# Kernel optimization log

Hardware: AMD Instinct MI355X
Metric: run time of the kernel (lower is better)

## Reference

```python
import jax, jax.numpy as jnp
import numpy as np

R_DISC = 0.05  # radius for discrepancy indicator
R_SIM = 0.03   # radius for sim/cross (indicator computed but unused downstream, as in source)
EPS = 1e-9


def setup_inputs() -> dict:
    key = jax.random.key(0)
    k1, k2, k3, k4 = jax.random.split(key, 4)
    bz, N, nsmp, K, C = 32, 16384, 4096, 64, 6
    features = jax.random.normal(k1, (bz, N, C), dtype=jnp.float32)
    nearest_k_idx = jax.random.randint(k2, (bz, nsmp, K), 0, N)
    # distances in [0, 0.06) so roughly half fall within r=0.03/0.05
    nearest_k_dist = jax.random.uniform(k3, (bz, nsmp, K), dtype=jnp.float32) * 0.06
    fps_idx = jax.random.randint(k4, (bz * nsmp,), 0, bz * N)
    return {"features": features, "nearest_k_idx": nearest_k_idx,
            "nearest_k_dist": nearest_k_dist, "fps_idx": fps_idx}


def _batched_index_select(features, idx):
    # features [bz,N,C], idx [bz,nsmp,K] -> [bz,nsmp,K,C]
    return jax.vmap(lambda f, i: f[i])(features, idx)


def _cos_sim_avg(feat_sub, nk_feat):
    # feat_sub [bz,nsmp,d], nk_feat [bz,nsmp,K,d] -> [bz,nsmp,1]
    num = jnp.sum(feat_sub[:, :, None, :] * nk_feat, axis=-1)
    den = jnp.maximum(jnp.linalg.norm(feat_sub, axis=-1)[:, :, None]
                      * jnp.linalg.norm(nk_feat, axis=-1), EPS)
    return jnp.mean(num / den, axis=-1, keepdims=True)


def reference(features, nearest_k_idx, nearest_k_dist, fps_idx):
    bz, N, C = features.shape
    nsmp = nearest_k_idx.shape[1]
    nk = _batched_index_select(features, nearest_k_idx)          # [bz,nsmp,K,C]
    feats_sub = features.reshape(bz * N, C)[fps_idx].reshape(bz, nsmp, C)

    # --- generate_feature_discrepancy (r=0.05): masked weighted neighbor mean ---
    ind = (nearest_k_dist <= R_DISC).astype(features.dtype)[..., None]  # [bz,nsmp,K,1]
    nk_avg = jnp.sum(nk * ind, axis=2) / jnp.sum(ind, axis=2)
    discrepancy = feats_sub - nk_avg                              # [bz,nsmp,C]

    # --- generate_feature_sim (r=0.03): mean cosine sim on xyz and normal splits ---
    sim = jnp.concatenate([_cos_sim_avg(feats_sub[:, :, :3], nk[:, :, :, :3]),
                           _cos_sim_avg(feats_sub[:, :, 3:], nk[:, :, :, 3:])],
                          axis=-1)                                # [bz,nsmp,2]

    # --- generate_feature_cross_prod: mean of feat_sub x neighbor over K ---
    cross = jnp.cross(feats_sub[:, :, None, :3], nk[:, :, :, :3])  # [bz,nsmp,K,3]
    cross_avg = jnp.mean(cross, axis=2)                            # [bz,nsmp,3]

    return jnp.concatenate([discrepancy, sim, cross_avg], axis=-1)  # [bz,nsmp,C+5]
```

## Files before the change

kernel.cpp:

```cpp
#include <hip/hip_runtime.h>

#define BZ    32
#define NPTS  16384
#define NSMP  4096
#define KNB   64
#define NCH   6
#define RDISC 0.05f


__global__ __launch_bounds__(64) void pnpp_kernel(
    const float* __restrict__ feat,
    const int*   __restrict__ nk_idx,
    const float* __restrict__ nk_dist,
    const int*   __restrict__ fps_idx,
    float*       __restrict__ out)
{
    const int lane = threadIdx.x & 63;
    const int bid  = blockIdx.x;
    const int work = (bid & 7) * (gridDim.x >> 3) + (bid >> 3);
    const int g = lane >> 2;
    const int j = lane & 3;
    const int s = work * 16 + g;
    const int b = s >> 12;

    const int p = fps_idx[s];
    const float* fsrow = feat + (long)p * NCH;
    const float4 fa  = *(const float4*)(fsrow);
    const float2 fb2 = *(const float2*)(fsrow + 4);
    const float fs0=fa.x, fs1=fa.y, fs2=fa.z, fs3=fa.w, fs4=fb2.x, fs5=fb2.y;
    const float qs1 = fs0*fs0 + fs1*fs1 + fs2*fs2;
    const float qs2 = fs3*fs3 + fs4*fs4 + fs5*fs5;

    const float* fbase = feat + (long)b * (NPTS * NCH);

    float cnt=0.f;
    float s0=0.f,s1=0.f,s2=0.f,s3=0.f,s4=0.f,s5=0.f;
    float m0=0.f,m1=0.f,m2=0.f;
    float c1=0.f,c2=0.f;

    const long kb0 = (long)s * KNB + j * 4;
    #pragma unroll
    for (int c = 0; c < 4; ++c) {
        const int4   i4 = *(const int4*)  (nk_idx  + kb0 + c * 16);
        const float4 d4 = *(const float4*)(nk_dist + kb0 + c * 16);
        const int   ridx[4] = {i4.x, i4.y, i4.z, i4.w};
        const float rdst[4] = {d4.x, d4.y, d4.z, d4.w};
        #pragma unroll
        for (int q = 0; q < 4; ++q) {
            const float* fr = fbase + (long)ridx[q] * NCH;
            const float4 fA = *(const float4*)(fr);
            const float2 fB = *(const float2*)(fr + 4);
            const float f0=fA.x, f1=fA.y, f2=fA.z, f3=fA.w, f4=fB.x, f5=fB.y;

            const float ind = (rdst[q] <= RDISC) ? 1.f : 0.f;
            cnt += ind;
            s0 += ind*f0; s1 += ind*f1; s2 += ind*f2;
            s3 += ind*f3; s4 += ind*f4; s5 += ind*f5;
            m0 += f0; m1 += f1; m2 += f2;

            const float q1 = f0*f0 + f1*f1 + f2*f2;
            const float n1 = fs0*f0 + fs1*f1 + fs2*f2;
            c1 += n1 * __builtin_amdgcn_rsqf(qs1 * q1);

            const float q2 = f3*f3 + f4*f4 + f5*f5;
            const float n2 = fs3*f3 + fs4*f4 + fs5*f5;
            c2 += n2 * __builtin_amdgcn_rsqf(qs2 * q2);
        }
    }

    #pragma unroll
    for (int m = 1; m < 4; m <<= 1) {
        cnt += __shfl_xor(cnt, m, 64);
        s0  += __shfl_xor(s0,  m, 64);
        s1  += __shfl_xor(s1,  m, 64);
        s2  += __shfl_xor(s2,  m, 64);
        s3  += __shfl_xor(s3,  m, 64);
        s4  += __shfl_xor(s4,  m, 64);
        s5  += __shfl_xor(s5,  m, 64);
        m0  += __shfl_xor(m0,  m, 64);
        m1  += __shfl_xor(m1,  m, 64);
        m2  += __shfl_xor(m2,  m, 64);
        c1  += __shfl_xor(c1,  m, 64);
        c2  += __shfl_xor(c2,  m, 64);
    }

    const float rc = __builtin_amdgcn_rcpf(cnt);
    const float d0 = fs0 - s0*rc, d1 = fs1 - s1*rc, d2 = fs2 - s2*rc;
    const float d3 = fs3 - s3*rc, d4 = fs4 - s4*rc, d5 = fs5 - s5*rc;
    const float ik = 1.f / (float)KNB;
    const float o6 = c1 * ik, o7 = c2 * ik;
    const float mm0 = m0 * ik, mm1 = m1 * ik, mm2 = m2 * ik;
    const float o8  = fs1*mm2 - fs2*mm1;
    const float o9  = fs2*mm0 - fs0*mm2;
    const float o10 = fs0*mm1 - fs1*mm0;

    const float v0 = (j==0) ? d0 : (j==1) ? d1 : (j==2) ? d2 : d3;
    const float v1 = (j==0) ? d4 : (j==1) ? d5 : (j==2) ? o6 : o7;
    const float v2 = (j==0) ? o8 : (j==1) ? o9 : o10;
    float* orow = out + (long)s * 11;
    orow[j]     = v0;
    orow[4 + j] = v1;
    if (j < 3) orow[8 + j] = v2;
}

extern "C" void kernel_launch(void* const* d_in, const int* in_sizes, int n_in,
                              void* d_out, int out_size, void* d_ws, size_t ws_size,
                              hipStream_t stream) {
    const float* feat = (const float*)d_in[0];
    const int*   nki  = (const int*)  d_in[1];
    const float* nkd  = (const float*)d_in[2];
    const int*   fps  = (const int*)  d_in[3];
    float* out = (float*)d_out;

    const int total_samples = BZ * NSMP;
    const int blocks = total_samples / 16;
    pnpp_kernel<<<dim3(blocks), dim3(64), 0, stream>>>(feat, nki, nkd, fps, out);
}
```

Baseline: 54.41 us.

## Split each neighbor row across lane pairs with single float4 gathers

Each sample now uses 8 lanes instead of 4. Lane pairs split the 6-channel neighbor row: the even lane loads channels 0-3 and the odd lane loads channels 2-5, each with one float4 gather, replacing a float4 plus float2 per lane, and each lane computes one of the two cosine terms. Results are rebuilt with extra xor shuffles. Blocks grow to 256 threads (4 waves) and index math moves from 64-bit to 32-bit. This halves per-lane gather and ALU work and doubles lane-level parallelism, at the cost of redundant loads of channels 2-3 and more shuffles.

```diff
diff --git a/kernel.cpp b/kernel.cpp
--- a/kernel.cpp
+++ b/kernel.cpp
@@ -8,7 +8,7 @@
 #define RDISC 0.05f
 
 
-__global__ __launch_bounds__(64) void pnpp_kernel(
+__global__ __launch_bounds__(256) void pnpp_kernel(
     const float* __restrict__ feat,
     const int*   __restrict__ nk_idx,
     const float* __restrict__ nk_dist,
@@ -16,91 +16,117 @@
     float*       __restrict__ out)
 {
     const int lane = threadIdx.x & 63;
+    const int wid  = threadIdx.x >> 6;
     const int bid  = blockIdx.x;
     const int work = (bid & 7) * (gridDim.x >> 3) + (bid >> 3);
-    const int g = lane >> 2;
-    const int j = lane & 3;
-    const int s = work * 16 + g;
+    const int g      = lane >> 3;
+    const int t      = lane & 7;
+    const int h      = t >> 1;
+    const int parity = t & 1;
+    const int s = work * 32 + wid * 8 + g;
     const int b = s >> 12;
 
     const int p = fps_idx[s];
-    const float* fsrow = feat + (long)p * NCH;
+    const float* fsrow = feat + p * NCH;
     const float4 fa  = *(const float4*)(fsrow);
     const float2 fb2 = *(const float2*)(fsrow + 4);
     const float fs0=fa.x, fs1=fa.y, fs2=fa.z, fs3=fa.w, fs4=fb2.x, fs5=fb2.y;
     const float qs1 = fs0*fs0 + fs1*fs1 + fs2*fs2;
     const float qs2 = fs3*fs3 + fs4*fs4 + fs5*fs5;
 
-    const float* fbase = feat + (long)b * (NPTS * NCH);
+    const float g0 = parity ? fs3 : fs0;
+    const float g1 = parity ? fs4 : fs1;
+    const float g2 = parity ? fs5 : fs2;
+    const float qsel = parity ? qs2 : qs1;
+
+    const float* fbase = feat + b * (NPTS * NCH) + parity * 2;
 
     float cnt=0.f;
-    float s0=0.f,s1=0.f,s2=0.f,s3=0.f,s4=0.f,s5=0.f;
-    float m0=0.f,m1=0.f,m2=0.f;
-    float c1=0.f,c2=0.f;
+    float A=0.f, B=0.f, C=0.f, D=0.f;
+    float mx=0.f, my=0.f, mz=0.f;
+    float cc=0.f;
 
-    const long kb0 = (long)s * KNB + j * 4;
+    const int kb = s * KNB + h * 16;
     #pragma unroll
     for (int c = 0; c < 4; ++c) {
-        const int4   i4 = *(const int4*)  (nk_idx  + kb0 + c * 16);
-        const float4 d4 = *(const float4*)(nk_dist + kb0 + c * 16);
+        const int4   i4 = *(const int4*)  (nk_idx  + kb + c * 4);
+        const float4 d4 = *(const float4*)(nk_dist + kb + c * 4);
         const int   ridx[4] = {i4.x, i4.y, i4.z, i4.w};
         const float rdst[4] = {d4.x, d4.y, d4.z, d4.w};
         #pragma unroll
         for (int q = 0; q < 4; ++q) {
-            const float* fr = fbase + (long)ridx[q] * NCH;
-            const float4 fA = *(const float4*)(fr);
-            const float2 fB = *(const float2*)(fr + 4);
-            const float f0=fA.x, f1=fA.y, f2=fA.z, f3=fA.w, f4=fB.x, f5=fB.y;
-
+            const float4 v = *(const float4*)(fbase + ridx[q] * NCH);
             const float ind = (rdst[q] <= RDISC) ? 1.f : 0.f;
             cnt += ind;
-            s0 += ind*f0; s1 += ind*f1; s2 += ind*f2;
-            s3 += ind*f3; s4 += ind*f4; s5 += ind*f5;
-            m0 += f0; m1 += f1; m2 += f2;
+            A += ind*v.x; B += ind*v.y; C += ind*v.z; D += ind*v.w;
+            mx += v.x; my += v.y; mz += v.z;
 
-            const float q1 = f0*f0 + f1*f1 + f2*f2;
-            const float n1 = fs0*f0 + fs1*f1 + fs2*f2;
-            c1 += n1 * __builtin_amdgcn_rsqf(qs1 * q1);
-
-            const float q2 = f3*f3 + f4*f4 + f5*f5;
-            const float n2 = fs3*f3 + fs4*f4 + fs5*f5;
-            c2 += n2 * __builtin_amdgcn_rsqf(qs2 * q2);
+            const float u  = parity ? v.y : v.x;
+            const float vv = parity ? v.z : v.y;
+            const float w  = parity ? v.w : v.z;
+            const float qq = u*u + vv*vv + w*w;
+            const float nn = g0*u + g1*vv + g2*w;
+            cc += nn * __builtin_amdgcn_rsqf(qsel * qq);
         }
     }
 
     #pragma unroll
-    for (int m = 1; m < 4; m <<= 1) {
+    for (int m = 2; m < 8; m <<= 1) {
         cnt += __shfl_xor(cnt, m, 64);
-        s0  += __shfl_xor(s0,  m, 64);
-        s1  += __shfl_xor(s1,  m, 64);
-        s2  += __shfl_xor(s2,  m, 64);
-        s3  += __shfl_xor(s3,  m, 64);
-        s4  += __shfl_xor(s4,  m, 64);
-        s5  += __shfl_xor(s5,  m, 64);
-        m0  += __shfl_xor(m0,  m, 64);
-        m1  += __shfl_xor(m1,  m, 64);
-        m2  += __shfl_xor(m2,  m, 64);
-        c1  += __shfl_xor(c1,  m, 64);
-        c2  += __shfl_xor(c2,  m, 64);
+        A   += __shfl_xor(A,   m, 64);
+        B   += __shfl_xor(B,   m, 64);
+        C   += __shfl_xor(C,   m, 64);
+        D   += __shfl_xor(D,   m, 64);
+        mx  += __shfl_xor(mx,  m, 64);
+        my  += __shfl_xor(my,  m, 64);
+        mz  += __shfl_xor(mz,  m, 64);
+        cc  += __shfl_xor(cc,  m, 64);
     }
+    const float pA  = __shfl_xor(A,  1, 64);
+    const float pB  = __shfl_xor(B,  1, 64);
+    const float pC  = __shfl_xor(C,  1, 64);
+    const float pD  = __shfl_xor(D,  1, 64);
+    const float pmx = __shfl_xor(mx, 1, 64);
+    const float pmy = __shfl_xor(my, 1, 64);
+    const float pmz = __shfl_xor(mz, 1, 64);
+    const float pcc = __shfl_xor(cc, 1, 64);
+
+    const float s0 = parity ? pA : A;
+    const float s1 = parity ? pB : B;
+    const float s2 = parity ? pC : C;
+    const float s3 = parity ? pD : D;
+    const float s4 = parity ? C  : pC;
+    const float s5 = parity ? D  : pD;
+    const float c1 = parity ? pcc : cc;
+    const float c2 = parity ? cc  : pcc;
+    const float Mx = parity ? pmx : mx;
+    const float My = parity ? pmy : my;
+    const float Mz = parity ? pmz : mz;
 
     const float rc = __builtin_amdgcn_rcpf(cnt);
     const float d0 = fs0 - s0*rc, d1 = fs1 - s1*rc, d2 = fs2 - s2*rc;
     const float d3 = fs3 - s3*rc, d4 = fs4 - s4*rc, d5 = fs5 - s5*rc;
     const float ik = 1.f / (float)KNB;
     const float o6 = c1 * ik, o7 = c2 * ik;
-    const float mm0 = m0 * ik, mm1 = m1 * ik, mm2 = m2 * ik;
-    const float o8  = fs1*mm2 - fs2*mm1;
-    const float o9  = fs2*mm0 - fs0*mm2;
-    const float o10 = fs0*mm1 - fs1*mm0;
+    const float ax = Mx * ik, ay = My * ik, az = Mz * ik;
+    const float o8  = fs1*az - fs2*ay;
+    const float o9  = fs2*ax - fs0*az;
+    const float o10 = fs0*ay - fs1*ax;
 
-    const float v0 = (j==0) ? d0 : (j==1) ? d1 : (j==2) ? d2 : d3;
-    const float v1 = (j==0) ? d4 : (j==1) ? d5 : (j==2) ? o6 : o7;
-    const float v2 = (j==0) ? o8 : (j==1) ? o9 : o10;
-    float* orow = out + (long)s * 11;
-    orow[j]     = v0;
-    orow[4 + j] = v1;
-    if (j < 3) orow[8 + j] = v2;
+    float v0 = d0;
+    v0 = (t == 1) ? d1 : v0;
+    v0 = (t == 2) ? d2 : v0;
+    v0 = (t == 3) ? d3 : v0;
+    v0 = (t == 4) ? d4 : v0;
+    v0 = (t == 5) ? d5 : v0;
+    v0 = (t == 6) ? o6 : v0;
+    v0 = (t == 7) ? o7 : v0;
+    float v1 = o8;
+    v1 = (t == 1) ? o9  : v1;
+    v1 = (t == 2) ? o10 : v1;
+    float* orow = out + s * 11;
+    orow[t] = v0;
+    if (t < 3) orow[8 + t] = v1;
 }
 
 extern "C" void kernel_launch(void* const* d_in, const int* in_sizes, int n_in,
@@ -113,6 +139,6 @@
     float* out = (float*)d_out;
 
     const int total_samples = BZ * NSMP;
-    const int blocks = total_samples / 16;
-    pnpp_kernel<<<dim3(blocks), dim3(64), 0, stream>>>(feat, nki, nkd, fps, out);
+    const int blocks = total_samples / 32;
+    pnpp_kernel<<<dim3(blocks), dim3(256), 0, stream>>>(feat, nki, nkd, fps, out);
 }
```

Result: faster. 50.82 us (-6.6%).

## Stage per-batch features into LDS as fp16 chunks and bucket neighbors by chunk

Applied to the files above, without the earlier changes.

Each 256-thread workgroup handles one thread per sample. It streams the batch's 16384-point feature table through LDS in 8 chunks of 2048 rows, converted to fp16, and sorts each sample's 64 neighbor indices into per-chunk buckets using packed byte counters. This swaps random global gathers for LDS reads, with the output staged through LDS so stores are coalesced. The cost is 8 block-wide syncs per workgroup, uneven per-thread bucket loops, and reduced precision in the neighbor features.

```diff
diff --git a/kernel.cpp b/kernel.cpp
--- a/kernel.cpp
+++ b/kernel.cpp
@@ -1,4 +1,5 @@
 #include <hip/hip_runtime.h>
+#include <hip/hip_fp16.h>
 
 #define BZ    32
 #define NPTS  16384
@@ -7,53 +8,120 @@
 #define NCH   6
 #define RDISC 0.05f
 
+#define NPASS 8
+#define CROWS 2048
+#define WGS   256
 
-__global__ __launch_bounds__(64) void pnpp_kernel(
+
+__global__ __launch_bounds__(256, 2) void pnpp_main(
     const float* __restrict__ feat,
     const int*   __restrict__ nk_idx,
     const float* __restrict__ nk_dist,
     const int*   __restrict__ fps_idx,
     float*       __restrict__ out)
 {
-    const int lane = threadIdx.x & 63;
-    const int bid  = blockIdx.x;
-    const int work = (bid & 7) * (gridDim.x >> 3) + (bid >> 3);
-    const int g = lane >> 2;
-    const int j = lane & 3;
-    const int s = work * 16 + g;
-    const int b = s >> 12;
+    __shared__ unsigned       hchunk[CROWS * 3];
+    __shared__ unsigned short ent[KNB * WGS];
 
-    const int p = fps_idx[s];
-    const float* fsrow = feat + (long)p * NCH;
+    const int tid = threadIdx.x;
+    const int wg0 = blockIdx.x * WGS;
+    const int s   = wg0 + tid;
+    const int b   = wg0 >> 12;
+    const float* fbatch = feat + (size_t)b * (NPTS * NCH);
+
+    unsigned er[32];
+    unsigned long long cnt = 0;
+    {
+        const int4*   ip = (const int4*)  (nk_idx  + (size_t)s * KNB);
+        const float4* dp = (const float4*)(nk_dist + (size_t)s * KNB);
+        #pragma unroll
+        for (int c = 0; c < 16; ++c) {
+            const int4   i4 = ip[c];
+            const float4 d4 = dp[c];
+            const unsigned e0 = (unsigned)i4.x | ((d4.x <= RDISC) ? 0x4000u : 0u);
+            const unsigned e1 = (unsigned)i4.y | ((d4.y <= RDISC) ? 0x4000u : 0u);
+            const unsigned e2 = (unsigned)i4.z | ((d4.z <= RDISC) ? 0x4000u : 0u);
+            const unsigned e3 = (unsigned)i4.w | ((d4.w <= RDISC) ? 0x4000u : 0u);
+            er[c * 2]     = e0 | (e1 << 16);
+            er[c * 2 + 1] = e2 | (e3 << 16);
+            cnt += 1ull << (((unsigned)i4.x >> 11) * 8);
+            cnt += 1ull << (((unsigned)i4.y >> 11) * 8);
+            cnt += 1ull << (((unsigned)i4.z >> 11) * 8);
+            cnt += 1ull << (((unsigned)i4.w >> 11) * 8);
+        }
+    }
+
+    unsigned long long cum = 0;
+    {
+        unsigned run = 0;
+        #pragma unroll
+        for (int b2 = 0; b2 < 8; ++b2) {
+            cum |= (unsigned long long)run << (b2 * 8);
+            run += (unsigned)((cnt >> (b2 * 8)) & 0xffULL);
+        }
+    }
+
+    const int pidx = fps_idx[s];
+    const float* fsrow = feat + (size_t)pidx * NCH;
     const float4 fa  = *(const float4*)(fsrow);
     const float2 fb2 = *(const float2*)(fsrow + 4);
-    const float fs0=fa.x, fs1=fa.y, fs2=fa.z, fs3=fa.w, fs4=fb2.x, fs5=fb2.y;
+    const float fs0 = fa.x, fs1 = fa.y, fs2 = fa.z;
+    const float fs3 = fa.w, fs4 = fb2.x, fs5 = fb2.y;
     const float qs1 = fs0*fs0 + fs1*fs1 + fs2*fs2;
     const float qs2 = fs3*fs3 + fs4*fs4 + fs5*fs5;
 
-    const float* fbase = feat + (long)b * (NPTS * NCH);
+    #define STAGE(PP)                                                          \
+    {                                                                          \
+        const float4* srcv = (const float4*)(fbatch) + (PP) * (CROWS*NCH/4);   \
+        _Pragma("unroll")                                                      \
+        for (int i = 0; i < 12; ++i) {                                         \
+            const float4 v = srcv[i * WGS + tid];                              \
+            const unsigned lo = (unsigned)__half_as_ushort(__float2half(v.x))  \
+                       | ((unsigned)__half_as_ushort(__float2half(v.y)) << 16);\
+            const unsigned hi = (unsigned)__half_as_ushort(__float2half(v.z))  \
+                       | ((unsigned)__half_as_ushort(__float2half(v.w)) << 16);\
+            *(uint2*)(&hchunk[(i * WGS + tid) * 2]) = make_uint2(lo, hi);      \
+        }                                                                      \
+    }
+    STAGE(0);
 
-    float cnt=0.f;
+    {
+        unsigned long long base = cum;
+        #pragma unroll
+        for (int k = 0; k < 64; ++k) {
+            const unsigned e  = (k & 1) ? (er[k >> 1] >> 16) : (er[k >> 1] & 0xffffu);
+            const unsigned bb = (e & 0x3fffu) >> 11;
+            const unsigned pos = (unsigned)((base >> (bb * 8)) & 0xffULL);
+            ent[pos * WGS + tid] = (unsigned short)e;
+            base += 1ull << (bb * 8);
+        }
+    }
+    __syncthreads();
+
+    float cntM = 0.f;
     float s0=0.f,s1=0.f,s2=0.f,s3=0.f,s4=0.f,s5=0.f;
     float m0=0.f,m1=0.f,m2=0.f;
     float c1=0.f,c2=0.f;
 
-    const long kb0 = (long)s * KNB + j * 4;
-    #pragma unroll
-    for (int c = 0; c < 4; ++c) {
-        const int4   i4 = *(const int4*)  (nk_idx  + kb0 + c * 16);
-        const float4 d4 = *(const float4*)(nk_dist + kb0 + c * 16);
-        const int   ridx[4] = {i4.x, i4.y, i4.z, i4.w};
-        const float rdst[4] = {d4.x, d4.y, d4.z, d4.w};
-        #pragma unroll
-        for (int q = 0; q < 4; ++q) {
-            const float* fr = fbase + (long)ridx[q] * NCH;
-            const float4 fA = *(const float4*)(fr);
-            const float2 fB = *(const float2*)(fr + 4);
-            const float f0=fA.x, f1=fA.y, f2=fA.z, f3=fA.w, f4=fB.x, f5=fB.y;
+    for (int p = 0; p < NPASS; ++p) {
+        unsigned cur  = (unsigned)((cum >> (p * 8)) & 0xffULL);
+        const unsigned endv = (p < 7) ? (unsigned)((cum >> (p * 8 + 8)) & 0xffULL) : 64u;
+        while (cur < endv) {
+            const unsigned e = ent[cur * WGS + tid];
+            ++cur;
+            const float ind = (e & 0x4000u) ? 1.f : 0.f;
+            const unsigned r = e & 0x7ffu;
+            const unsigned u0 = hchunk[3*r + 0];
+            const unsigned u1 = hchunk[3*r + 1];
+            const unsigned u2 = hchunk[3*r + 2];
+            const float f0 = __half2float(__ushort_as_half((unsigned short)(u0 & 0xffffu)));
+            const float f1 = __half2float(__ushort_as_half((unsigned short)(u0 >> 16)));
+            const float f2 = __half2float(__ushort_as_half((unsigned short)(u1 & 0xffffu)));
+            const float f3 = __half2float(__ushort_as_half((unsigned short)(u1 >> 16)));
+            const float f4 = __half2float(__ushort_as_half((unsigned short)(u2 & 0xffffu)));
+            const float f5 = __half2float(__ushort_as_half((unsigned short)(u2 >> 16)));
 
-            const float ind = (rdst[q] <= RDISC) ? 1.f : 0.f;
-            cnt += ind;
+            cntM += ind;
             s0 += ind*f0; s1 += ind*f1; s2 += ind*f2;
             s3 += ind*f3; s4 += ind*f4; s5 += ind*f5;
             m0 += f0; m1 += f1; m2 += f2;
@@ -61,46 +129,44 @@
             const float q1 = f0*f0 + f1*f1 + f2*f2;
             const float n1 = fs0*f0 + fs1*f1 + fs2*f2;
             c1 += n1 * __builtin_amdgcn_rsqf(qs1 * q1);
-
             const float q2 = f3*f3 + f4*f4 + f5*f5;
             const float n2 = fs3*f3 + fs4*f4 + fs5*f5;
             c2 += n2 * __builtin_amdgcn_rsqf(qs2 * q2);
         }
+        __syncthreads();
+        if (p + 1 < NPASS) {
+            STAGE(p + 1);
+            __syncthreads();
+        }
     }
 
-    #pragma unroll
-    for (int m = 1; m < 4; m <<= 1) {
-        cnt += __shfl_xor(cnt, m, 64);
-        s0  += __shfl_xor(s0,  m, 64);
-        s1  += __shfl_xor(s1,  m, 64);
-        s2  += __shfl_xor(s2,  m, 64);
-        s3  += __shfl_xor(s3,  m, 64);
-        s4  += __shfl_xor(s4,  m, 64);
-        s5  += __shfl_xor(s5,  m, 64);
-        m0  += __shfl_xor(m0,  m, 64);
-        m1  += __shfl_xor(m1,  m, 64);
-        m2  += __shfl_xor(m2,  m, 64);
-        c1  += __shfl_xor(c1,  m, 64);
-        c2  += __shfl_xor(c2,  m, 64);
-    }
-
-    const float rc = __builtin_amdgcn_rcpf(cnt);
+    const float rc = __builtin_amdgcn_rcpf(cntM);
     const float d0 = fs0 - s0*rc, d1 = fs1 - s1*rc, d2 = fs2 - s2*rc;
     const float d3 = fs3 - s3*rc, d4 = fs4 - s4*rc, d5 = fs5 - s5*rc;
     const float ik = 1.f / (float)KNB;
     const float o6 = c1 * ik, o7 = c2 * ik;
-    const float mm0 = m0 * ik, mm1 = m1 * ik, mm2 = m2 * ik;
-    const float o8  = fs1*mm2 - fs2*mm1;
-    const float o9  = fs2*mm0 - fs0*mm2;
-    const float o10 = fs0*mm1 - fs1*mm0;
+    const float ax = m0 * ik, ay = m1 * ik, az = m2 * ik;
+    const float o8  = fs1*az - fs2*ay;
+    const float o9  = fs2*ax - fs0*az;
+    const float o10 = fs0*ay - fs1*ax;
 
-    const float v0 = (j==0) ? d0 : (j==1) ? d1 : (j==2) ? d2 : d3;
-    const float v1 = (j==0) ? d4 : (j==1) ? d5 : (j==2) ? o6 : o7;
-    const float v2 = (j==0) ? o8 : (j==1) ? o9 : o10;
-    float* orow = out + (long)s * 11;
-    orow[j]     = v0;
-    orow[4 + j] = v1;
-    if (j < 3) orow[8 + j] = v2;
+    float* ostage = (float*)(void*)hchunk;
+    ostage[tid * 11 + 0]  = d0;
+    ostage[tid * 11 + 1]  = d1;
+    ostage[tid * 11 + 2]  = d2;
+    ostage[tid * 11 + 3]  = d3;
+    ostage[tid * 11 + 4]  = d4;
+    ostage[tid * 11 + 5]  = d5;
+    ostage[tid * 11 + 6]  = o6;
+    ostage[tid * 11 + 7]  = o7;
+    ostage[tid * 11 + 8]  = o8;
+    ostage[tid * 11 + 9]  = o9;
+    ostage[tid * 11 + 10] = o10;
+    __syncthreads();
+    const size_t obase = (size_t)wg0 * 11;
+    #pragma unroll
+    for (int i = 0; i < 11; ++i)
+        out[obase + i * WGS + tid] = ostage[i * WGS + tid];
 }
 
 extern "C" void kernel_launch(void* const* d_in, const int* in_sizes, int n_in,
@@ -112,7 +178,6 @@
     const int*   fps  = (const int*)  d_in[3];
     float* out = (float*)d_out;
 
-    const int total_samples = BZ * NSMP;
-    const int blocks = total_samples / 16;
-    pnpp_kernel<<<dim3(blocks), dim3(64), 0, stream>>>(feat, nki, nkd, fps, out);
+    const int blocks = (BZ * NSMP) / WGS;
+    pnpp_main<<<dim3(blocks), dim3(WGS), 0, stream>>>(feat, nki, nkd, fps, out);
 }
```

Result: slower. 70.58 us (+29.7%).
